# Kernel optimization log

Measured on AMD Instinct MI355X. Metric: run time of the kernel, lower is better.

The kernel has to match this reference:

```python
import jax, jax.numpy as jnp
import numpy as np

B, S, N, D, NAMED, NTYPES = 8, 64, 100, 1024, 768, 5

def _ln(x, g, b, eps=1e-5):
    m = x.mean(-1, keepdims=True)
    v = ((x - m) ** 2).mean(-1, keepdims=True)
    return (x - m) * jax.lax.rsqrt(v + eps) * g + b

def _lin(x, W, b=None):
    y = x @ W.T
    return y if b is None else y + b

def setup_inputs():
    key = jax.random.key(0)
    ks = jax.random.split(key, 24)
    p = lambda i, shape, s=0.02: jax.random.normal(ks[i], shape, jnp.float32) * s
    inp = {}
    inp['scene_reps'] = jax.random.normal(ks[0], (B, S, D), jnp.float32)
    u = jax.random.uniform(ks[1], (B, N, S))
    keep = (jax.random.uniform(ks[2], (B, N, S)) < 0.25).astype(jnp.float32)
    inp['incidence_matrix'] = u * keep
    inp['edge_type_ids'] = jax.random.randint(ks[3], (B, S), 0, NTYPES)
    inp['entity_type_ids'] = jax.random.randint(ks[4], (B, N), 0, NTYPES)
    inp['entity_mask'] = jax.random.uniform(ks[5], (B, N)) < 0.9
    inp['entity_name_embs'] = jax.random.normal(ks[6], (B, N, NAMED), jnp.float32)
    inp['type_embed'] = p(7, (NTYPES, D), 1.0)
    inp['name_W'] = p(8, (D, NAMED))
    inp['name_ln_g'] = jnp.ones(D); inp['name_ln_b'] = jnp.zeros(D)
    inp['n2e_W'] = p(9, (D, D)); inp['n2e_b'] = jnp.zeros(D)
    inp['t2e_W'] = p(10, (D, D)); inp['t2e_b'] = jnp.zeros(D)
    inp['edge_ln_g'] = jnp.ones(D); inp['edge_ln_b'] = jnp.zeros(D)
    inp['gate_W1'] = p(11, (D // 4, D)); inp['gate_b1'] = jnp.zeros(D // 4)
    inp['gate_W2'] = p(12, (3, D // 4)); inp['gate_b2'] = jnp.zeros(3)
    inp['ms_W'] = p(13, (D, D)); inp['ms_b'] = jnp.zeros(D)
    inp['ma_W'] = p(14, (D, D)); inp['ma_b'] = jnp.zeros(D)
    inp['mi_W'] = p(15, (D, D)); inp['mi_b'] = jnp.zeros(D)
    inp['role_w'] = p(16, (D,))
    inp['gru_Wih'] = p(17, (3 * D, D)); inp['gru_Whh'] = p(18, (3 * D, D))
    inp['gru_bih'] = jnp.zeros(3 * D); inp['gru_bhh'] = jnp.zeros(3 * D)
    inp['upd_ln_g'] = jnp.ones(D); inp['upd_ln_b'] = jnp.zeros(D)
    inp['eo_W'] = p(19, (D, D)); inp['eo_b'] = jnp.zeros(D)
    inp['eo_ln_g'] = jnp.ones(D); inp['eo_ln_b'] = jnp.zeros(D)
    inp['res_ln_g'] = jnp.ones(D); inp['res_ln_b'] = jnp.zeros(D)
    return inp

def reference(scene_reps, incidence_matrix, edge_type_ids, entity_type_ids, entity_mask, entity_name_embs, type_embed, name_W, name_ln_g, name_ln_b, n2e_W, n2e_b, t2e_W, t2e_b, edge_ln_g, edge_ln_b, gate_W1, gate_b1, gate_W2, gate_b2, ms_W, ms_b, ma_W, ma_b, mi_W, mi_b, role_w, gru_Wih, gru_Whh, gru_bih, gru_bhh, upd_ln_g, upd_ln_b, eo_W, eo_b, eo_ln_g, eo_ln_b, res_ln_g, res_ln_b):
    # edge_type_ids is accepted by the torch module but unused in its forward.
    dt = scene_reps.dtype
    emaskf = entity_mask.astype(dt)  # [B,N]
    h0 = type_embed[entity_type_ids] + _ln(_lin(entity_name_embs, name_W), name_ln_g, name_ln_b)
    h0 = h0 * emaskf[..., None]
    eye = jnp.eye(N, dtype=dt)
    step_ids = jnp.arange(S)

    def step(carry, xs):
        h, ebuf = carry  # h [B,N,D], ebuf [B,S,D] (hyperedge history)
        s, x_s, inc_s = xs  # x_s [B,D], inc_s [B,N]
        roles = inc_s * emaskf
        wsum = jnp.maximum(roles.sum(1, keepdims=True), 1.0)
        mean_ent = jnp.einsum('bn,bnd->bd', roles, h) / wsum
        e_s = _ln(_lin(mean_ent, n2e_W, n2e_b) + _lin(x_s, t2e_W, t2e_b), edge_ln_g, edge_ln_b)
        in_mask = (roles > 0).astype(dt)[..., None]  # [B,N,1]
        msg_scene = _lin(e_s, ms_W, ms_b)[:, None, :]
        # arc stream: attention over past hyperedges with exponential recency decay
        valid = (step_ids < s).astype(dt)
        denom = jnp.maximum(s - 1, 1).astype(dt)
        decay = jnp.exp(-1.0 + step_ids.astype(dt) / denom) * valid  # linspace(-1,0,s)
        arc = incidence_matrix * roles[:, :, None] * decay[None, None, :]  # [B,N,S]
        arc = arc / jnp.maximum(arc.sum(-1, keepdims=True), 1e-8)
        msg_arc = _lin(jnp.einsum('bns,bsd->bnd', arc, jax.lax.stop_gradient(ebuf)), ma_W, ma_b)
        msg_arc = jnp.where(s > 0, msg_arc, jnp.zeros_like(msg_arc))
        # interaction stream: entity co-occurrence within the scene
        co = roles[:, :, None] * roles[:, None, :] * (1.0 - eye)
        co = co / jnp.maximum(co.sum(-1, keepdims=True), 1e-8)
        msg_int = _lin(jnp.einsum('bnm,bmd->bnd', co, h), mi_W, mi_b)
        gate = jax.nn.softmax(_lin(jax.nn.gelu(_lin(e_s, gate_W1, gate_b1), approximate=False), gate_W2, gate_b2), axis=-1)  # [B,3]
        msg = gate[:, 0, None, None] * msg_scene + gate[:, 1, None, None] * msg_arc + gate[:, 2, None, None] * msg_int
        msg = msg + (roles[..., None] * role_w) * in_mask
        # GRUCell (torch semantics) + LayerNorm, masked update
        gi = _lin(msg, gru_Wih, gru_bih)
        gh = _lin(h, gru_Whh, gru_bhh)
        i_r, i_z, i_n = jnp.split(gi, 3, axis=-1)
        h_r, h_z, h_n = jnp.split(gh, 3, axis=-1)
        r = jax.nn.sigmoid(i_r + h_r)
        z = jax.nn.sigmoid(i_z + h_z)
        n = jnp.tanh(i_n + r * h_n)
        h_new = jnp.clip(_ln((1 - z) * n + z * h, upd_ln_g, upd_ln_b), -50.0, 50.0)
        h = h * (1 - in_mask) + h_new * in_mask
        ebuf = ebuf.at[:, s].set(e_s)
        return (h, ebuf), e_s

    ebuf0 = jnp.zeros((B, S, D), dt)
    (h_fin, _), es = jax.lax.scan(step, (h0, ebuf0), (step_ids, scene_reps.transpose(1, 0, 2), incidence_matrix.transpose(2, 0, 1)))
    H = es.transpose(1, 0, 2)  # [B,S,D]
    H = _ln(H + scene_reps, res_ln_g, res_ln_b)
    H = _ln(jax.nn.gelu(_lin(H, eo_W, eo_b), approximate=False), eo_ln_g, eo_ln_b)
    return (H, h_fin)
```

## Files before the change

kernel.cpp:

```cpp
#include <hip/hip_runtime.h>
#include <math.h>

#define B_   8
#define S_   64
#define N_   100
#define D_   1024
#define ND_  768
#define BN_  800
#define G3_  3072
#define G6_  6144
#define HC7  7168
#define RSC  0.00390625f

typedef _Float16 f16x8 __attribute__((ext_vector_type(8)));
typedef float f32x4 __attribute__((ext_vector_type(4)));

#define MFMA16(a,b,c) __builtin_amdgcn_mfma_f32_16x16x32_f16(a, b, c, 0, 0, 0)

static __device__ __forceinline__ float wave_sum(float v) {
    for (int off = 32; off > 0; off >>= 1) v += __shfl_down(v, off, 64);
    return v;
}

static __device__ __forceinline__ float wave_allsum(float v) {
    for (int off = 1; off < 64; off <<= 1) v += __shfl_xor(v, off, 64);
    return v;
}

static __device__ __forceinline__ float block_sum(float v) {
    __shared__ float red_[8];
    float w = wave_sum(v);
    int lane = threadIdx.x & 63, wid = threadIdx.x >> 6;
    __syncthreads();
    if (lane == 0) red_[wid] = w;
    __syncthreads();
    float t = 0.f;
    for (int i = 0; i < 4; ++i) t += red_[i];
    return t;
}

static __device__ __forceinline__ float gelu_f(float x) {
    return 0.5f * x * (1.f + erff(x * 0.70710678118654752f));
}

static __device__ __forceinline__ unsigned short f2h(float x) {
    union { _Float16 h; unsigned short u; } c; c.h = (_Float16)x; return c.u;
}

__global__ __launch_bounds__(256) void k_f2h(
    const float* __restrict__ src, unsigned short* __restrict__ dst,
    int rows, int cols, int ldd)
{
    size_t n = (size_t)rows * cols;
    size_t i = ((size_t)blockIdx.x * 256 + threadIdx.x) * 4;
    if (i >= n) return;
    int r = (int)(i / cols);
    int c = (int)(i - (size_t)r * cols);
    float4 v = *(const float4*)(src + i);
    ushort4 o; o.x = f2h(v.x); o.y = f2h(v.y); o.z = f2h(v.z); o.w = f2h(v.w);
    *(ushort4*)(dst + (size_t)r * ldd + c) = o;
}

__global__ __launch_bounds__(256) void k_f2hT(
    const float* __restrict__ src, unsigned short* __restrict__ dst,
    int R, int C, int ldd, int rowoff)
{
    __shared__ _Float16 T[32][33];
    int tr = threadIdx.x >> 3, tc4 = (threadIdx.x & 7) * 4;
    int r0 = blockIdx.y * 32, c0 = blockIdx.x * 32;
    float4 v = *(const float4*)(src + (size_t)(r0 + tr) * C + c0 + tc4);
    T[tc4][tr] = (_Float16)v.x; T[tc4+1][tr] = (_Float16)v.y;
    T[tc4+2][tr] = (_Float16)v.z; T[tc4+3][tr] = (_Float16)v.w;
    __syncthreads();
    union { _Float16 h; unsigned short u; } cv;
    ushort4 o;
    cv.h = T[tr][tc4];   o.x = cv.u;
    cv.h = T[tr][tc4+1]; o.y = cv.u;
    cv.h = T[tr][tc4+2]; o.z = cv.u;
    cv.h = T[tr][tc4+3]; o.w = cv.u;
    *(ushort4*)(dst + (size_t)(rowoff + c0 + tr) * ldd + r0 + tc4) = o;
}

__global__ __launch_bounds__(256) void k_mfma16_nt(
    const unsigned short* __restrict__ A16, const unsigned short* __restrict__ W16,
    const float* __restrict__ bias, float* __restrict__ C,
    unsigned short* __restrict__ C16, float oscale,
    int M, int Nc, int K)
{
    int m0 = blockIdx.y * 64; if (m0 >= M) return;
    int n0 = blockIdx.x * 128;
    __shared__ _Float16 sA[64][72];
    __shared__ _Float16 sB[128][72];
    int tid = threadIdx.x;
    int w = tid >> 6, l = tid & 63;
    int l15 = l & 15, q = l >> 4;
    int wn = w * 32;
    int arow = tid >> 3, achk = (tid & 7) * 8;
    f32x4 acc[4][2] = {};
    for (int k0 = 0; k0 < K; k0 += 64) {
        for (int ri = 0; ri < 64; ri += 32) {
            int gm = m0 + arow + ri;
            uint4 v = make_uint4(0u, 0u, 0u, 0u);
            if (gm < M) v = *(const uint4*)(A16 + (size_t)gm * K + k0 + achk);
            *(uint4*)(&sA[arow + ri][achk]) = v;
        }
        for (int i = 0; i < 4; ++i) {
            int r = arow + 32 * i;
            *(uint4*)(&sB[r][achk]) = *(const uint4*)(W16 + (size_t)(n0 + r) * K + k0 + achk);
        }
        __syncthreads();
#pragma unroll
        for (int ks = 0; ks < 64; ks += 32) {
            f16x8 b0 = *(const f16x8*)(&sB[wn + l15][ks + q*8]);
            f16x8 b1 = *(const f16x8*)(&sB[wn + 16 + l15][ks + q*8]);
#pragma unroll
            for (int mi = 0; mi < 4; ++mi) {
                f16x8 a = *(const f16x8*)(&sA[mi*16 + l15][ks + q*8]);
                acc[mi][0] = MFMA16(a, b0, acc[mi][0]);
                acc[mi][1] = MFMA16(a, b1, acc[mi][1]);
            }
        }
        __syncthreads();
    }
    for (int mi = 0; mi < 4; ++mi)
        for (int nj = 0; nj < 2; ++nj)
            for (int r = 0; r < 4; ++r) {
                int gm = m0 + mi*16 + q*4 + r;
                int cl = wn + nj*16 + l15;
                if (gm < M) {
                    size_t off = (size_t)gm * Nc + n0 + cl;
                    float v = acc[mi][nj][r];
                    if (C16) C16[off] = f2h(v * oscale);
                    else C[off] = v + (bias ? bias[n0 + cl] : 0.f);
                }
            }
}

__global__ __launch_bounds__(256) void k_h0(
    const float* __restrict__ P, const int* __restrict__ etype,
    const int* __restrict__ emask, const float* __restrict__ temb,
    const float* __restrict__ g, const float* __restrict__ bt,
    float* __restrict__ h, unsigned short* __restrict__ h16)
{
    int bn = blockIdx.x, tid = threadIdx.x;
    int t = etype[bn], mk = emask[bn];
    float x[4]; float lsum = 0.f;
    for (int k = 0; k < 4; ++k) { x[k] = P[(size_t)bn*D_ + tid + 256*k]; lsum += x[k]; }
    float mean = block_sum(lsum) * (1.f / D_);
    float lv = 0.f;
    for (int k = 0; k < 4; ++k) { float d = x[k] - mean; lv += d * d; }
    float inv = rsqrtf(block_sum(lv) * (1.f / D_) + 1e-5f);
    for (int k = 0; k < 4; ++k) {
        int d = tid + 256*k;
        float y = (x[k] - mean) * inv * g[d] + bt[d];
        float hv = mk ? (temb[(size_t)t*D_ + d] + y) : 0.f;
        h[(size_t)bn*D_ + d] = hv;
        h16[(size_t)bn*D_ + d] = f2h(hv);
    }
}

__global__ __launch_bounds__(256) void k_hcat0(
    const unsigned short* __restrict__ h16, const unsigned short* __restrict__ n2e16,
    const unsigned short* __restrict__ Wmi16, const unsigned short* __restrict__ Whh16,
    float* __restrict__ Hcat)
{
    int m0 = blockIdx.y * 32;
    int n0 = blockIdx.x * 64;
    const unsigned short* Bp; int ldb; int nl;
    if (n0 < 1024)      { Bp = n2e16;        ldb = D_;  nl = n0; }
    else if (n0 < 4096) { Bp = Wmi16 + 2048; ldb = G3_; nl = n0 - 1024; }
    else                { Bp = Whh16;        ldb = D_;  nl = n0 - 4096; }
    __shared__ _Float16 sA[32][72];
    __shared__ _Float16 sB[64][72];
    int tid = threadIdx.x;
    int w = tid >> 6, l = tid & 63;
    int l15 = l & 15, q = l >> 4;
    int wm = (w & 1) * 16, wn = (w >> 1) * 32;
    int arow = tid >> 3, achk = (tid & 7) * 8;
    int gmA = m0 + arow;
    f32x4 acc[2] = {};
    for (int k0 = 0; k0 < D_; k0 += 64) {
        *(uint4*)(&sA[arow][achk]) = *(const uint4*)(h16 + (size_t)gmA*D_ + k0 + achk);
        *(uint4*)(&sB[arow][achk])      = *(const uint4*)(Bp + (size_t)(nl + arow)*ldb + k0 + achk);
        *(uint4*)(&sB[arow + 32][achk]) = *(const uint4*)(Bp + (size_t)(nl + arow + 32)*ldb + k0 + achk);
        __syncthreads();
#pragma unroll
        for (int ks = 0; ks < 64; ks += 32) {
            f16x8 a  = *(const f16x8*)(&sA[wm + l15][ks + q*8]);
            f16x8 b0 = *(const f16x8*)(&sB[wn + l15][ks + q*8]);
            f16x8 b1 = *(const f16x8*)(&sB[wn + 16 + l15][ks + q*8]);
            acc[0] = MFMA16(a, b0, acc[0]);
            acc[1] = MFMA16(a, b1, acc[1]);
        }
        __syncthreads();
    }
    for (int j = 0; j < 2; ++j)
        for (int r = 0; r < 4; ++r) {
            int row = wm + q*4 + r;
            Hcat[(size_t)(m0 + row)*HC7 + n0 + wn + j*16 + l15] = acc[j][r];
        }
}

__global__ __launch_bounds__(256) void k_front(
    const float* __restrict__ inc, const int* __restrict__ emask,
    const float* __restrict__ Esmi, float* __restrict__ arcsum,
    int* __restrict__ cntp, int* __restrict__ lst, float* __restrict__ rro,
    float* __restrict__ scl,
    const int* __restrict__ prevcnt, const int* __restrict__ prevlist,
    const unsigned short* __restrict__ h16, const unsigned short* __restrict__ n2e16,
    const unsigned short* __restrict__ Wmi16, const unsigned short* __restrict__ Whh16,
    float* __restrict__ Hcat, float* __restrict__ gatepre,
    float* __restrict__ esumP, float* __restrict__ TmiP, float* __restrict__ wsumP,
    int s)
{
    int tid = threadIdx.x, bid = blockIdx.x;
    if (bid == 0 && tid < 32) gatepre[tid] = 0.f;
    if (bid < BN_) {
        int m = bid;
        int b = m / N_;
        float r = emask[m] ? inc[(size_t)m*S_ + s] : 0.f;
        if (r <= 0.f) return;
        __shared__ int sidx, nwa;
        __shared__ float wav[S_]; __shared__ int wai[S_];
        if (tid == 0) { sidx = atomicAdd(cntp, 1); nwa = 0; }
        __syncthreads();
        int idx = sidx;
        float denomA = fmaxf((float)(s - 1), 1.f);
        float wa = 0.f;
        if (tid < s) {
            float iv = inc[(size_t)m*S_ + tid];
            if (iv > 0.f) {
                wa = iv * r * expf(-1.f + (float)tid / denomA);
                int p = atomicAdd(&nwa, 1);
                wav[p] = wa; wai[p] = tid;
            }
        }
        float dA = block_sum(wa);
        float rm = 0.f;
        if (tid < N_) rm = emask[b*N_ + tid] ? inc[((size_t)b*N_ + tid)*S_ + s] : 0.f;
        float wsum = block_sum(rm);
        __syncthreads();
        int na = nwa;
        float sclA = 1.f / fmaxf(dA, 1e-8f);
        if (tid == 0) {
            lst[idx] = m; rro[idx] = r;
            scl[idx] = r / fmaxf(r * (wsum - r), 1e-8f);
            wsumP[b] = wsum;
        }
        float rprev = (s > 0) ? inc[(size_t)m*S_ + (s-1)] : 0.f;
        if (rprev <= 0.f) {
            const float4* hp = (const float4*)(Hcat + (size_t)m*HC7);
#pragma unroll
            for (int j2 = 0; j2 < 4; ++j2) {
                float4 hv = hp[tid + 256*j2];
                int c = (tid + 256*j2) * 4;
                float* dst = (c < 1024) ? (esumP + (size_t)b*D_ + c)
                                        : (TmiP + (size_t)b*G3_ + (c - 1024));
                atomicAdd(dst + 0, r*hv.x); atomicAdd(dst + 1, r*hv.y);
                atomicAdd(dst + 2, r*hv.z); atomicAdd(dst + 3, r*hv.w);
            }
        }
        float a12[12];
#pragma unroll
        for (int k = 0; k < 12; ++k) a12[k] = 0.f;
        for (int j = 0; j < na; ++j) {
            float wj = wav[j];
            const float* ep = Esmi + ((size_t)b*S_ + wai[j])*G3_;
#pragma unroll
            for (int k = 0; k < 12; ++k) a12[k] += wj * ep[tid + 256*k];
        }
        float* ao = arcsum + (size_t)idx*G3_;
#pragma unroll
        for (int k = 0; k < 12; ++k) ao[tid + 256*k] = a12[k] * sclA;
    } else {
        int pM = *prevcnt;
        int t = bid - BN_;
        int nt = t % 112, mt = t / 112;
        int m0 = mt * 64;
        if (m0 >= pM) return;
        int n0 = nt * 64;
        const unsigned short* Bp; int ldb; int nl;
        if (n0 < 1024)      { Bp = n2e16;        ldb = D_;  nl = n0; }
        else if (n0 < 4096) { Bp = Wmi16 + 2048; ldb = G3_; nl = n0 - 1024; }
        else                { Bp = Whh16;        ldb = D_;  nl = n0 - 4096; }
        __shared__ _Float16 sA[64][72];
        __shared__ _Float16 sB[64][72];
        __shared__ int slist[64];
        __shared__ float srn[64];
        __shared__ int sbb[64];
        if (tid < 64) {
            int gm = m0 + tid;
            int m = (gm < pM) ? prevlist[gm] : 0;
            slist[tid] = m;
            float rn = 0.f;
            if (gm < pM) rn = emask[m] ? inc[(size_t)m*S_ + s] : 0.f;
            srn[tid] = rn;
            sbb[tid] = m / N_;
        }
        __syncthreads();
        int w = tid >> 6, l = tid & 63;
        int l15 = l & 15, q = l >> 4;
        int wm = (w & 1) * 32, wn = (w >> 1) * 32;
        int arow = tid >> 3, achk = (tid & 7) * 8;
        f32x4 acc[2][2] = {};
        for (int k0 = 0; k0 < D_; k0 += 64) {
            for (int ri = 0; ri < 64; ri += 32) {
                int row = arow + ri, gm = m0 + row;
                uint4 v = make_uint4(0u,0u,0u,0u);
                if (gm < pM) v = *(const uint4*)(h16 + (size_t)slist[row]*D_ + k0 + achk);
                *(uint4*)(&sA[row][achk]) = v;
            }
            *(uint4*)(&sB[arow][achk])      = *(const uint4*)(Bp + (size_t)(nl + arow)*ldb + k0 + achk);
            *(uint4*)(&sB[arow + 32][achk]) = *(const uint4*)(Bp + (size_t)(nl + arow + 32)*ldb + k0 + achk);
            __syncthreads();
#pragma unroll
            for (int ks = 0; ks < 64; ks += 32) {
                f16x8 a0 = *(const f16x8*)(&sA[wm + l15][ks + q*8]);
                f16x8 a1 = *(const f16x8*)(&sA[wm + 16 + l15][ks + q*8]);
                f16x8 b0 = *(const f16x8*)(&sB[wn + l15][ks + q*8]);
                f16x8 b1 = *(const f16x8*)(&sB[wn + 16 + l15][ks + q*8]);
                acc[0][0] = MFMA16(a0, b0, acc[0][0]);
                acc[0][1] = MFMA16(a0, b1, acc[0][1]);
                acc[1][0] = MFMA16(a1, b0, acc[1][0]);
                acc[1][1] = MFMA16(a1, b1, acc[1][1]);
            }
            __syncthreads();
        }
        for (int mi = 0; mi < 2; ++mi)
            for (int nj = 0; nj < 2; ++nj)
                for (int r = 0; r < 4; ++r) {
                    int row = wm + mi*16 + q*4 + r;
                    int gm = m0 + row;
                    if (gm < pM) {
                        float v = acc[mi][nj][r];
                        int c = n0 + wn + nj*16 + l15;
                        Hcat[(size_t)slist[row]*HC7 + c] = v;
                        float rn = srn[row];
                        if (rn > 0.f && c < 4096) {
                            float* dst = (c < 1024)
                                ? (esumP + (size_t)sbb[row]*D_ + c)
                                : (TmiP + (size_t)sbb[row]*G3_ + (c - 1024));
                            atomicAdd(dst, rn * v);
                        }
                    }
                }
    }
}

__global__ __launch_bounds__(256) void k_mid(
    const float* __restrict__ esumP, const float* __restrict__ wsumP,
    float* __restrict__ esumZ, float* __restrict__ TmiZ, float* __restrict__ wsumZ,
    const float* __restrict__ n2eb, const float* __restrict__ pre_t2e,
    const float* __restrict__ elng, const float* __restrict__ elnb,
    const float* __restrict__ gW1, const float* __restrict__ gb1,
    const float* __restrict__ gW2, const unsigned short* __restrict__ Wmi16,
    float* __restrict__ esbuf, float* __restrict__ gatepre,
    float* __restrict__ Emi, float* __restrict__ Esmi,
    int* __restrict__ ctrl, int par, int s)
{
    int bid = blockIdx.x, tid = threadIdx.x;
    if (bid < 32) {
        __shared__ float se[D_];
        int b = bid >> 2, seg = bid & 3;
        if (bid == 0 && tid == 0) ctrl[1 - par] = 0;
        esumZ[(size_t)b*D_ + seg*256 + tid] = 0.f;
#pragma unroll
        for (int j = 0; j < 3; ++j) TmiZ[(size_t)b*G3_ + seg*768 + j*256 + tid] = 0.f;
        if (seg == 0 && tid == 0) wsumZ[b] = 0.f;
        float invw = 1.f / fmaxf(wsumP[b], 1.f);
        float4 ev = ((const float4*)(esumP + (size_t)b*D_))[tid];
        float4 nb = ((const float4*)n2eb)[tid];
        float4 pt = ((const float4*)(pre_t2e + ((size_t)b*S_ + s)*D_))[tid];
        float x[4] = { ev.x*invw + nb.x + pt.x, ev.y*invw + nb.y + pt.y,
                       ev.z*invw + nb.z + pt.z, ev.w*invw + nb.w + pt.w };
        float mean = block_sum(x[0]+x[1]+x[2]+x[3]) * (1.f / D_);
        float lv = 0.f;
#pragma unroll
        for (int k = 0; k < 4; ++k) { float d = x[k] - mean; lv += d * d; }
        float inv = rsqrtf(block_sum(lv) * (1.f / D_) + 1e-5f);
        float4 lg = ((const float4*)elng)[tid];
        float4 lb = ((const float4*)elnb)[tid];
        float y0 = (x[0]-mean)*inv*lg.x + lb.x;
        float y1 = (x[1]-mean)*inv*lg.y + lb.y;
        float y2 = (x[2]-mean)*inv*lg.z + lb.z;
        float y3 = (x[3]-mean)*inv*lg.w + lb.w;
        int d4 = tid * 4;
        se[d4] = y0; se[d4+1] = y1; se[d4+2] = y2; se[d4+3] = y3;
        if (seg == 0)
            ((float4*)(esbuf + ((size_t)b*S_ + s)*D_))[tid] = make_float4(y0,y1,y2,y3);
        __syncthreads();
        if (tid < 64) {
            int u = seg * 64 + tid;
            float acc = gb1[u];
            const float* w1 = gW1 + (size_t)u * D_;
            for (int j = 0; j < D_; j += 4) {
                float4 w = *(const float4*)(w1 + j);
                acc += w.x*se[j] + w.y*se[j+1] + w.z*se[j+2] + w.w*se[j+3];
            }
            float hg = gelu_f(acc);
            for (int c = 0; c < 3; ++c) {
                float p = wave_sum(gW2[c*256 + u] * hg);
                if (tid == 0) atomicAdd(gatepre + b*4 + c, p);
            }
        }
    } else {
        __shared__ float se32[8][1028];
        int w = tid >> 6, lane = tid & 63;
        for (int bb = 0; bb < 2; ++bb) {
            int b = w*2 + bb;
            float invw = 1.f / fmaxf(wsumP[b], 1.f);
            int d0 = lane * 16;
            const float4* ep = (const float4*)(esumP + (size_t)b*D_ + d0);
            const float4* np = (const float4*)(n2eb + d0);
            const float4* pp = (const float4*)(pre_t2e + ((size_t)b*S_ + s)*D_ + d0);
            float x[16]; float sm = 0.f;
#pragma unroll
            for (int j = 0; j < 4; ++j) {
                float4 e = ep[j], n = np[j], p = pp[j];
                x[j*4+0] = e.x*invw + n.x + p.x;
                x[j*4+1] = e.y*invw + n.y + p.y;
                x[j*4+2] = e.z*invw + n.z + p.z;
                x[j*4+3] = e.w*invw + n.w + p.w;
                sm += x[j*4+0] + x[j*4+1] + x[j*4+2] + x[j*4+3];
            }
            float mean = wave_allsum(sm) * (1.f / D_);
            float lv = 0.f;
#pragma unroll
            for (int j = 0; j < 16; ++j) { float d = x[j] - mean; lv += d * d; }
            float inv = rsqrtf(wave_allsum(lv) * (1.f / D_) + 1e-5f);
            const float4* lgp = (const float4*)(elng + d0);
            const float4* lbp = (const float4*)(elnb + d0);
#pragma unroll
            for (int j = 0; j < 4; ++j) {
                float4 lg = lgp[j], lb = lbp[j];
                se32[b][d0 + j*4 + 0] = (x[j*4+0]-mean)*inv*lg.x + lb.x;
                se32[b][d0 + j*4 + 1] = (x[j*4+1]-mean)*inv*lg.y + lb.y;
                se32[b][d0 + j*4 + 2] = (x[j*4+2]-mean)*inv*lg.z + lb.z;
                se32[b][d0 + j*4 + 3] = (x[j*4+3]-mean)*inv*lg.w + lb.w;
            }
        }
        __syncthreads();
        int c0 = (bid - 32) * 32;
        int colg = tid >> 5, t31 = tid & 31;
        int cb = c0 + colg * 4;
        float accA[4][8] = {};
        float accB[4][8] = {};
#pragma unroll
        for (int i = 0; i < 8; ++i) {
            int kh = t31*4 + i*128;
            float wf[4][4];
#pragma unroll
            for (int c = 0; c < 4; ++c) {
                union { uint2 u; _Float16 h[4]; } cv;
                cv.u = *(const uint2*)(Wmi16 + (size_t)(cb + c)*G3_ + kh);
                wf[c][0] = (float)cv.h[0]; wf[c][1] = (float)cv.h[1];
                wf[c][2] = (float)cv.h[2]; wf[c][3] = (float)cv.h[3];
            }
#pragma unroll
            for (int b = 0; b < 8; ++b) {
                float4 sv = *(const float4*)(&se32[b][kh]);
#pragma unroll
                for (int c = 0; c < 4; ++c)
                    accA[c][b] += wf[c][0]*sv.x + wf[c][1]*sv.y
                                + wf[c][2]*sv.z + wf[c][3]*sv.w;
            }
        }
#pragma unroll
        for (int i = 0; i < 8; ++i) {
            int kh = t31*4 + i*128;
            float wf[4][4];
#pragma unroll
            for (int c = 0; c < 4; ++c) {
                union { uint2 u; _Float16 h[4]; } cv;
                cv.u = *(const uint2*)(Wmi16 + (size_t)(cb + c)*G3_ + 1024 + kh);
                wf[c][0] = (float)cv.h[0]; wf[c][1] = (float)cv.h[1];
                wf[c][2] = (float)cv.h[2]; wf[c][3] = (float)cv.h[3];
            }
#pragma unroll
            for (int b = 0; b < 8; ++b) {
                float4 sv = *(const float4*)(&se32[b][kh]);
#pragma unroll
                for (int c = 0; c < 4; ++c)
                    accB[c][b] += wf[c][0]*sv.x + wf[c][1]*sv.y
                                + wf[c][2]*sv.z + wf[c][3]*sv.w;
            }
        }
#pragma unroll
        for (int off = 16; off >= 1; off >>= 1) {
#pragma unroll
            for (int c = 0; c < 4; ++c)
#pragma unroll
                for (int b = 0; b < 8; ++b) {
                    accA[c][b] += __shfl_down(accA[c][b], off, 32);
                    accB[c][b] += __shfl_down(accB[c][b], off, 32);
                }
        }
        if (t31 == 0) {
#pragma unroll
            for (int c = 0; c < 4; ++c) {
                int col = cb + c;
#pragma unroll
                for (int b = 0; b < 8; ++b) {
                    Emi[(size_t)b*G3_ + col] = accA[c][b];
                    Esmi[((size_t)b*S_ + s)*G3_ + col] = accB[c][b];
                }
            }
        }
    }
}

__global__ __launch_bounds__(256) void k_fin(
    const int* __restrict__ lst, const int* __restrict__ cntp,
    const float* __restrict__ rro, const float* __restrict__ scl,
    const float* __restrict__ gatepre, const float* __restrict__ gb2,
    const float* __restrict__ Hcat, const float* __restrict__ Emi,
    const float* __restrict__ arcsum, const float* __restrict__ Tmi,
    const float* __restrict__ gBm, const float* __restrict__ bih,
    const float* __restrict__ bhh,
    const float* __restrict__ ulng, const float* __restrict__ ulnb,
    float* __restrict__ h, unsigned short* __restrict__ h16, int s)
{
    int row = blockIdx.x;
    if (row >= *cntp) return;
    int bn = lst[row];
    int b = bn / N_;
    int tid = threadIdx.x;
    float t0 = gatepre[b*4+0] + gb2[0];
    float t1 = gatepre[b*4+1] + gb2[1];
    float t2 = gatepre[b*4+2] + gb2[2];
    float mx = fmaxf(t0, fmaxf(t1, t2));
    float e0 = expf(t0-mx), e1 = expf(t1-mx), e2 = expf(t2-mx);
    float si = 1.f / (e0 + e1 + e2);
    float g0 = e0*si, g1 = (s > 0) ? e1*si : 0.f, g2 = e2*si;
    float rv = rro[row];
    float sI = scl[row];
    const float* Hrow = Hcat + (size_t)bn * HC7;
    const float* em = Emi + (size_t)b * G3_;
    const float* as = arcsum + (size_t)row * G3_;
    const float* tm = Tmi + (size_t)b * G3_;
    float u[4]; float lsum = 0.f;
    for (int k = 0; k < 4; ++k) {
        int d = tid + 256*k;
        float ip[3];
#pragma unroll
        for (int c = 0; c < 3; ++c) {
            int dd = c*D_ + d;
            float gint = tm[dd] - rv * Hrow[1024 + dd];
            ip[c] = RSC * (g0*em[dd] + g1*as[dd] + g2*sI*gint)
                  + g0*gBm[dd] + g1*gBm[G3_ + dd] + g2*gBm[2*G3_ + dd]
                  + rv*gBm[3*G3_ + dd] + bih[dd];
        }
        float hr = Hrow[4096 + d]        + bhh[d];
        float hz = Hrow[4096 + D_ + d]   + bhh[D_ + d];
        float hn = Hrow[4096 + 2*D_ + d] + bhh[2*D_ + d];
        float hv = h[(size_t)bn*D_ + d];
        float r = 1.f / (1.f + expf(-(ip[0] + hr)));
        float z = 1.f / (1.f + expf(-(ip[1] + hz)));
        float nn = tanhf(ip[2] + r * hn);
        u[k] = (1.f - z) * nn + z * hv;
        lsum += u[k];
    }
    float mean = block_sum(lsum) * (1.f / D_);
    float lv = 0.f;
    for (int k = 0; k < 4; ++k) { float d = u[k] - mean; lv += d * d; }
    float inv = rsqrtf(block_sum(lv) * (1.f / D_) + 1e-5f);
    for (int k = 0; k < 4; ++k) {
        int d = tid + 256*k;
        float y = (u[k] - mean) * inv * ulng[d] + ulnb[d];
        y = fminf(fmaxf(y, -50.f), 50.f);
        h[(size_t)bn*D_ + d] = y;
        h16[(size_t)bn*D_ + d] = f2h(y);
    }
}

__global__ __launch_bounds__(256) void k_resln(
    float* __restrict__ buf, const float* __restrict__ scene,
    const float* __restrict__ g, const float* __restrict__ bt,
    unsigned short* __restrict__ H16)
{
    size_t row = blockIdx.x;
    int tid = threadIdx.x;
    float x[4]; float lsum = 0.f;
    for (int k = 0; k < 4; ++k) {
        int d = tid + 256*k;
        x[k] = buf[row*D_ + d] + scene[row*D_ + d];
        lsum += x[k];
    }
    float mean = block_sum(lsum) * (1.f / D_);
    float lv = 0.f;
    for (int k = 0; k < 4; ++k) { float d = x[k] - mean; lv += d * d; }
    float inv = rsqrtf(block_sum(lv) * (1.f / D_) + 1e-5f);
    for (int k = 0; k < 4; ++k) {
        int d = tid + 256*k;
        float y = (x[k] - mean) * inv * g[d] + bt[d];
        buf[row*D_ + d] = y;
        H16[row*D_ + d] = f2h(y);
    }
}

__global__ __launch_bounds__(256) void k_final(
    const float* __restrict__ G, const float* __restrict__ g, const float* __restrict__ bt,
    float* __restrict__ outH, const float* __restrict__ h, float* __restrict__ outh)
{
    int tid = threadIdx.x;
    if (blockIdx.x < B_*S_) {
        size_t row = blockIdx.x;
        float x[4]; float lsum = 0.f;
        for (int k = 0; k < 4; ++k) {
            x[k] = gelu_f(G[row*D_ + tid + 256*k]);
            lsum += x[k];
        }
        float mean = block_sum(lsum) * (1.f / D_);
        float lv = 0.f;
        for (int k = 0; k < 4; ++k) { float d = x[k] - mean; lv += d * d; }
        float inv = rsqrtf(block_sum(lv) * (1.f / D_) + 1e-5f);
        for (int k = 0; k < 4; ++k) {
            int d = tid + 256*k;
            outH[row*D_ + d] = (x[k] - mean) * inv * g[d] + bt[d];
        }
    } else {
        size_t bn = blockIdx.x - B_*S_;
        for (int d = tid; d < D_; d += 256)
            outh[bn*D_ + d] = h[bn*D_ + d];
    }
}

extern "C" void kernel_launch(void* const* d_in, const int* in_sizes, int n_in,
                              void* d_out, int out_size, void* d_ws, size_t ws_size,
                              hipStream_t stream)
{
    const float* scene = (const float*)d_in[0];
    const float* inc   = (const float*)d_in[1];
    const int*   etype = (const int*)d_in[3];
    const int*   emask = (const int*)d_in[4];
    const float* nemb  = (const float*)d_in[5];
    const float* temb  = (const float*)d_in[6];
    const float* nameW = (const float*)d_in[7];
    const float* nlg   = (const float*)d_in[8];
    const float* nlb   = (const float*)d_in[9];
    const float* n2eW  = (const float*)d_in[10];
    const float* n2eb  = (const float*)d_in[11];
    const float* t2eW  = (const float*)d_in[12];
    const float* t2eb  = (const float*)d_in[13];
    const float* elng  = (const float*)d_in[14];
    const float* elnb  = (const float*)d_in[15];
    const float* gW1   = (const float*)d_in[16];
    const float* gb1   = (const float*)d_in[17];
    const float* gW2   = (const float*)d_in[18];
    const float* gb2   = (const float*)d_in[19];
    const float* msW   = (const float*)d_in[20];
    const float* msB   = (const float*)d_in[21];
    const float* maW   = (const float*)d_in[22];
    const float* maB   = (const float*)d_in[23];
    const float* miW   = (const float*)d_in[24];
    const float* miB   = (const float*)d_in[25];
    const float* rolew = (const float*)d_in[26];
    const float* Wih   = (const float*)d_in[27];
    const float* Whh   = (const float*)d_in[28];
    const float* bih   = (const float*)d_in[29];
    const float* bhh   = (const float*)d_in[30];
    const float* ulng  = (const float*)d_in[31];
    const float* ulnb  = (const float*)d_in[32];
    const float* eoW   = (const float*)d_in[33];
    const float* eoB   = (const float*)d_in[34];
    const float* eolng = (const float*)d_in[35];
    const float* eolnb = (const float*)d_in[36];
    const float* rlng  = (const float*)d_in[37];
    const float* rlnb  = (const float*)d_in[38];

    float* outH = (float*)d_out;
    float* outh = outH + (size_t)B_*S_*D_;

    float* W = (float*)d_ws;
    size_t o = 0;
    int*   ctrl     = (int*)(W + o); o += 64;
    float* esum2    = W + o; o += 2*(size_t)B_*D_;
    float* Tmi2     = W + o; o += 2*(size_t)B_*G3_;
    float* wsum2    = W + o; o += 16;
    float* gatepre  = W + o; o += 32;
    float* rowrole  = W + o; o += 2*BN_;
    float* sclbuf   = W + o; o += BN_;
    int*   list     = (int*)(W + o); o += 2*BN_;
    float* hbuf     = W + o; o += (size_t)BN_*D_;
    float* Hcat     = W + o; o += (size_t)BN_*HC7;
    float* pre_t2e  = W + o; o += (size_t)B_*S_*D_;
    float* gBm      = W + o; o += 4*G3_;
    float* Emi      = W + o; o += (size_t)B_*G3_;
    float* Esmi     = W + o; o += (size_t)B_*S_*G3_;
    float* arcsum   = W + o; o += (size_t)BN_*G3_;
    float* tmp      = W + o; o += (size_t)BN_*D_;
    unsigned short* U = (unsigned short*)(W + o);
    size_t uo = 0;
    unsigned short* h16    = U + uo; uo += (size_t)BN_*D_;
    unsigned short* H16    = U + uo; uo += (size_t)B_*S_*D_;
    unsigned short* Wih16  = U + uo; uo += (size_t)G3_*D_;
    unsigned short* Whh16  = U + uo; uo += (size_t)G3_*D_;
    unsigned short* n2e16  = U + uo; uo += (size_t)D_*D_;
    unsigned short* eoW16  = U + uo; uo += (size_t)D_*D_;
    unsigned short* nW16   = U + uo; uo += (size_t)D_*ND_;
    unsigned short* nE16   = U + uo; uo += (size_t)BN_*ND_;
    unsigned short* t2e16  = U + uo; uo += (size_t)D_*D_;
    unsigned short* sc16   = U + uo; uo += (size_t)B_*S_*D_;
    unsigned short* WcatT16= U + uo; uo += (size_t)G3_*D_;
    unsigned short* Wmi16  = U + uo; uo += (size_t)G3_*G3_;
    unsigned short* bias4  = U + uo; uo += 4*D_;

    hipMemsetAsync(ctrl, 0,
        (64 + 2*(size_t)B_*D_ + 2*(size_t)B_*G3_ + 16) * sizeof(float), stream);

    #define CVT(src, dst, r, c, ld) \
        k_f2h<<<(((size_t)(r)*(c)/4 + 255)/256), 256, 0, stream>>>(src, dst, r, c, ld)
    CVT(Wih,   Wih16, G3_, D_,  D_);
    CVT(Whh,   Whh16, G3_, D_,  D_);
    CVT(n2eW,  n2e16, D_,  D_,  D_);
    CVT(nameW, nW16,  D_,  ND_, ND_);
    CVT(nemb,  nE16,  BN_, ND_, ND_);
    CVT(eoW,   eoW16, D_,  D_,  D_);
    CVT(t2eW,  t2e16, D_,  D_,  D_);
    CVT(scene, sc16,  B_*S_, D_, D_);
    CVT(msB,   bias4 + 0,    1, D_, D_);
    CVT(maB,   bias4 + D_,   1, D_, D_);
    CVT(miB,   bias4 + 2*D_, 1, D_, D_);
    CVT(rolew, bias4 + 3*D_, 1, D_, D_);
    #undef CVT
    k_f2hT<<<dim3(32,32), 256, 0, stream>>>(msW, WcatT16, D_, D_, D_, 0);
    k_f2hT<<<dim3(32,32), 256, 0, stream>>>(maW, WcatT16, D_, D_, D_, D_);
    k_f2hT<<<dim3(32,32), 256, 0, stream>>>(miW, WcatT16, D_, D_, D_, 2*D_);

    k_mfma16_nt<<<dim3(G3_/128, G3_/64), 256, 0, stream>>>(
        Wih16, WcatT16, nullptr, nullptr, Wmi16, 256.f, G3_, G3_, D_);
    k_mfma16_nt<<<dim3(G3_/128, 1), 256, 0, stream>>>(
        bias4, Wih16, nullptr, gBm, nullptr, 1.f, 4, G3_, D_);
    k_mfma16_nt<<<dim3(D_/128, (B_*S_+63)/64), 256, 0, stream>>>(
        sc16, t2e16, t2eb, pre_t2e, nullptr, 1.f, B_*S_, D_, D_);
    k_mfma16_nt<<<dim3(D_/128, (BN_+63)/64), 256, 0, stream>>>(
        nE16, nW16, nullptr, tmp, nullptr, 1.f, BN_, D_, ND_);
    k_h0<<<BN_, 256, 0, stream>>>(tmp, etype, emask, temb, nlg, nlb, hbuf, h16);
    k_hcat0<<<dim3(112, 25), 256, 0, stream>>>(h16, n2e16, Wmi16, Whh16, Hcat);

    for (int s = 0; s < S_; ++s) {
        int par = s & 1;
        int*   cntp = ctrl + par;
        int*   pcnt = ctrl + (1 - par);
        int*   lst  = list + par * BN_;
        int*   plst = list + (1 - par) * BN_;
        float* rro  = rowrole + par * BN_;
        float* esumP = esum2 + (size_t)par * B_*D_;
        float* esumZ = esum2 + (size_t)(1 - par) * B_*D_;
        float* TmiP  = Tmi2 + (size_t)par * B_*G3_;
        float* TmiZ  = Tmi2 + (size_t)(1 - par) * B_*G3_;
        float* wsumP = wsum2 + par * 8;
        float* wsumZ = wsum2 + (1 - par) * 8;
        k_front<<<BN_ + 112*13, 256, 0, stream>>>(inc, emask, Esmi, arcsum,
            cntp, lst, rro, sclbuf, pcnt, plst, h16, n2e16, Wmi16, Whh16,
            Hcat, gatepre, esumP, TmiP, wsumP, s);
        k_mid<<<128, 256, 0, stream>>>(esumP, wsumP, esumZ, TmiZ, wsumZ,
            n2eb, pre_t2e, elng, elnb, gW1, gb1, gW2, Wmi16,
            outH, gatepre, Emi, Esmi, ctrl, par, s);
        k_fin<<<BN_, 256, 0, stream>>>(lst, cntp, rro, sclbuf, gatepre, gb2,
            Hcat, Emi, arcsum, TmiP, gBm, bih, bhh, ulng, ulnb, hbuf, h16, s);
    }

    k_resln<<<B_*S_, 256, 0, stream>>>(outH, scene, rlng, rlnb, H16);
    k_mfma16_nt<<<dim3(D_/128, (B_*S_+63)/64), 256, 0, stream>>>(
        H16, eoW16, eoB, tmp, nullptr, 1.f, B_*S_, D_, D_);
    k_final<<<B_*S_ + BN_, 256, 0, stream>>>(tmp, eolng, eolnb, outH, hbuf, outh);
}
```

Before: 4.203 ms.

## Fuse per-step recurrent kernels into one persistent cooperative kernel with grid syncs

Replaces the 64-step loop of three kernel launches (front, mid, fin) with a single persistent cooperative kernel that loops over steps. Each former kernel becomes a phase, and grid.sync() separates the phases. The grid is capped at 512 blocks, and each block strides over that phase's tasks. The aim is to remove about 192 kernel launches and their launch gaps. In exchange, occupancy and parallelism per phase are limited to the co-resident grid, and grid-wide barrier costs are added. If cooperative launch fails, the code falls back to the original multi-launch loop.

```diff
diff --git a/kernel.cpp b/kernel.cpp
--- a/kernel.cpp
+++ b/kernel.cpp
@@ -1,4 +1,5 @@
 #include <hip/hip_runtime.h>
+#include <hip/hip_cooperative_groups.h>
 #include <math.h>
 
 #define B_   8
@@ -8,12 +9,14 @@
 #define ND_  768
 #define BN_  800
 #define G3_  3072
-#define G6_  6144
 #define HC7  7168
+#define NBLK 512
 #define RSC  0.00390625f
 
 typedef _Float16 f16x8 __attribute__((ext_vector_type(8)));
 typedef float f32x4 __attribute__((ext_vector_type(4)));
+
+namespace cg = cooperative_groups;
 
 #define MFMA16(a,b,c) __builtin_amdgcn_mfma_f32_16x16x32_f16(a, b, c, 0, 0, 0)
 
@@ -570,6 +573,394 @@
         y = fminf(fmaxf(y, -50.f), 50.f);
         h[(size_t)bn*D_ + d] = y;
         h16[(size_t)bn*D_ + d] = f2h(y);
+    }
+}
+
+struct LoopA {
+    const float* inc; const int* emask;
+    float* Esmi; float* arcsum;
+    int* ctrl; int* list2; float* rro2; float* scl;
+    unsigned short* h16; float* hbuf;
+    const unsigned short* n2e16; const unsigned short* Wmi16; const unsigned short* Whh16;
+    float* Hcat; float* gatepre;
+    float* esum2; float* Tmi2; float* wsum2;
+    const float* pre_t2e; float* Emi; float* esbuf;
+    const float* n2eb; const float* elng; const float* elnb;
+    const float* gW1; const float* gb1; const float* gW2; const float* gb2;
+    const float* gBm; const float* bih; const float* bhh;
+    const float* ulng; const float* ulnb;
+};
+
+union SMu {
+    struct { _Float16 A[64][72]; _Float16 Bm[64][72]; int slist[64]; float srn[64]; int sbb[64]; } g;
+    struct { float se32[8][1028]; } e;
+    struct { float se1[D_]; } t;
+    struct { float wav[S_]; int wai[S_]; } r;
+};
+
+__global__ __launch_bounds__(256, 2) void k_loop(LoopA a)
+{
+    cg::grid_group grid = cg::this_grid();
+    __shared__ SMu sm;
+    __shared__ int sh_i0, sh_i1;
+    int tid = threadIdx.x;
+    int bid = blockIdx.x;
+    int gdim = gridDim.x;
+
+    for (int s = 0; s < S_; ++s) {
+        int par = s & 1;
+        int* cntp = a.ctrl + par;
+        const int* pcnt = a.ctrl + (1 - par);
+        int* lst = a.list2 + par * BN_;
+        const int* plst = a.list2 + (1 - par) * BN_;
+        float* rro = a.rro2 + par * BN_;
+        float* esumP = a.esum2 + (size_t)par * B_ * D_;
+        float* esumZ = a.esum2 + (size_t)(1 - par) * B_ * D_;
+        float* TmiP  = a.Tmi2 + (size_t)par * B_ * G3_;
+        float* TmiZ  = a.Tmi2 + (size_t)(1 - par) * B_ * G3_;
+        const float* wsumP = a.wsum2 + par * 8;
+        float* wsumPw = a.wsum2 + par * 8;
+        float* wsumZ = a.wsum2 + (1 - par) * 8;
+
+        for (int tk = bid; tk < BN_ + 112*13; tk += gdim) {
+            __syncthreads();
+            if (tk < BN_) {
+                if (tk == 0 && tid < 32) a.gatepre[tid] = 0.f;
+                int m = tk, b = m / N_;
+                float r = a.emask[m] ? a.inc[(size_t)m*S_ + s] : 0.f;
+                if (r > 0.f) {
+                    if (tid == 0) { sh_i0 = atomicAdd(cntp, 1); sh_i1 = 0; }
+                    __syncthreads();
+                    int idx = sh_i0;
+                    float denomA = fmaxf((float)(s - 1), 1.f);
+                    float wa = 0.f;
+                    if (tid < s) {
+                        float iv = a.inc[(size_t)m*S_ + tid];
+                        if (iv > 0.f) {
+                            wa = iv * r * expf(-1.f + (float)tid / denomA);
+                            int p = atomicAdd(&sh_i1, 1);
+                            sm.r.wav[p] = wa; sm.r.wai[p] = tid;
+                        }
+                    }
+                    float dA = block_sum(wa);
+                    float rm = 0.f;
+                    if (tid < N_) rm = a.emask[b*N_ + tid] ? a.inc[((size_t)b*N_ + tid)*S_ + s] : 0.f;
+                    float wsum = block_sum(rm);
+                    __syncthreads();
+                    int na = sh_i1;
+                    float sclA = 1.f / fmaxf(dA, 1e-8f);
+                    if (tid == 0) {
+                        lst[idx] = m; rro[idx] = r;
+                        a.scl[idx] = r / fmaxf(r * (wsum - r), 1e-8f);
+                        wsumPw[b] = wsum;
+                    }
+                    float rprev = (s > 0) ? a.inc[(size_t)m*S_ + (s-1)] : 0.f;
+                    if (rprev <= 0.f) {
+                        const float4* hp = (const float4*)(a.Hcat + (size_t)m*HC7);
+#pragma unroll
+                        for (int j2 = 0; j2 < 4; ++j2) {
+                            float4 hv = hp[tid + 256*j2];
+                            int c = (tid + 256*j2) * 4;
+                            float* dst = (c < 1024) ? (esumP + (size_t)b*D_ + c)
+                                                    : (TmiP + (size_t)b*G3_ + (c - 1024));
+                            atomicAdd(dst + 0, r*hv.x); atomicAdd(dst + 1, r*hv.y);
+                            atomicAdd(dst + 2, r*hv.z); atomicAdd(dst + 3, r*hv.w);
+                        }
+                    }
+                    float a12[12];
+#pragma unroll
+                    for (int k = 0; k < 12; ++k) a12[k] = 0.f;
+                    for (int j = 0; j < na; ++j) {
+                        float wj = sm.r.wav[j];
+                        const float* ep = a.Esmi + ((size_t)b*S_ + sm.r.wai[j])*G3_;
+#pragma unroll
+                        for (int k = 0; k < 12; ++k) a12[k] += wj * ep[tid + 256*k];
+                    }
+                    float* ao = a.arcsum + (size_t)idx*G3_;
+#pragma unroll
+                    for (int k = 0; k < 12; ++k) ao[tid + 256*k] = a12[k] * sclA;
+                }
+            } else {
+                int pM = *pcnt;
+                int t = tk - BN_;
+                int nt = t % 112, mt = t / 112;
+                int m0 = mt * 64;
+                if (m0 < pM) {
+                    int n0 = nt * 64;
+                    const unsigned short* Bp; int ldb; int nl;
+                    if (n0 < 1024)      { Bp = a.n2e16;        ldb = D_;  nl = n0; }
+                    else if (n0 < 4096) { Bp = a.Wmi16 + 2048; ldb = G3_; nl = n0 - 1024; }
+                    else                { Bp = a.Whh16;        ldb = D_;  nl = n0 - 4096; }
+                    if (tid < 64) {
+                        int gm = m0 + tid;
+                        int m = (gm < pM) ? plst[gm] : 0;
+                        sm.g.slist[tid] = m;
+                        float rn = 0.f;
+                        if (gm < pM) rn = a.emask[m] ? a.inc[(size_t)m*S_ + s] : 0.f;
+                        sm.g.srn[tid] = rn;
+                        sm.g.sbb[tid] = m / N_;
+                    }
+                    __syncthreads();
+                    int w = tid >> 6, l = tid & 63;
+                    int l15 = l & 15, q = l >> 4;
+                    int wm = (w & 1) * 32, wn = (w >> 1) * 32;
+                    int arow = tid >> 3, achk = (tid & 7) * 8;
+                    f32x4 acc[2][2] = {};
+                    for (int k0 = 0; k0 < D_; k0 += 64) {
+                        for (int ri = 0; ri < 64; ri += 32) {
+                            int row = arow + ri, gm = m0 + row;
+                            uint4 v = make_uint4(0u,0u,0u,0u);
+                            if (gm < pM) v = *(const uint4*)(a.h16 + (size_t)sm.g.slist[row]*D_ + k0 + achk);
+                            *(uint4*)(&sm.g.A[row][achk]) = v;
+                        }
+                        *(uint4*)(&sm.g.Bm[arow][achk])      = *(const uint4*)(Bp + (size_t)(nl + arow)*ldb + k0 + achk);
+                        *(uint4*)(&sm.g.Bm[arow + 32][achk]) = *(const uint4*)(Bp + (size_t)(nl + arow + 32)*ldb + k0 + achk);
+                        __syncthreads();
+#pragma unroll
+                        for (int ks = 0; ks < 64; ks += 32) {
+                            f16x8 a0 = *(const f16x8*)(&sm.g.A[wm + l15][ks + q*8]);
+                            f16x8 a1 = *(const f16x8*)(&sm.g.A[wm + 16 + l15][ks + q*8]);
+                            f16x8 b0 = *(const f16x8*)(&sm.g.Bm[wn + l15][ks + q*8]);
+                            f16x8 b1 = *(const f16x8*)(&sm.g.Bm[wn + 16 + l15][ks + q*8]);
+                            acc[0][0] = MFMA16(a0, b0, acc[0][0]);
+                            acc[0][1] = MFMA16(a0, b1, acc[0][1]);
+                            acc[1][0] = MFMA16(a1, b0, acc[1][0]);
+                            acc[1][1] = MFMA16(a1, b1, acc[1][1]);
+                        }
+                        __syncthreads();
+                    }
+                    for (int mi = 0; mi < 2; ++mi)
+                        for (int nj = 0; nj < 2; ++nj)
+                            for (int r4 = 0; r4 < 4; ++r4) {
+                                int row = wm + mi*16 + q*4 + r4;
+                                int gm = m0 + row;
+                                if (gm < pM) {
+                                    float v = acc[mi][nj][r4];
+                                    int c = n0 + wn + nj*16 + l15;
+                                    a.Hcat[(size_t)sm.g.slist[row]*HC7 + c] = v;
+                                    float rn = sm.g.srn[row];
+                                    if (rn > 0.f && c < 4096) {
+                                        float* dst = (c < 1024)
+                                            ? (esumP + (size_t)sm.g.sbb[row]*D_ + c)
+                                            : (TmiP + (size_t)sm.g.sbb[row]*G3_ + (c - 1024));
+                                        atomicAdd(dst, rn * v);
+                                    }
+                                }
+                            }
+                }
+            }
+        }
+        grid.sync();
+
+        for (int tk = bid; tk < 128; tk += gdim) {
+            __syncthreads();
+            if (tk < 32) {
+                int b = tk >> 2, seg = tk & 3;
+                if (tk == 0 && tid == 0) a.ctrl[1 - par] = 0;
+                esumZ[(size_t)b*D_ + seg*256 + tid] = 0.f;
+#pragma unroll
+                for (int j = 0; j < 3; ++j) TmiZ[(size_t)b*G3_ + seg*768 + j*256 + tid] = 0.f;
+                if (seg == 0 && tid == 0) wsumZ[b] = 0.f;
+                float invw = 1.f / fmaxf(wsumP[b], 1.f);
+                float4 ev = ((const float4*)(esumP + (size_t)b*D_))[tid];
+                float4 nb = ((const float4*)a.n2eb)[tid];
+                float4 pt = ((const float4*)(a.pre_t2e + ((size_t)b*S_ + s)*D_))[tid];
+                float x[4] = { ev.x*invw + nb.x + pt.x, ev.y*invw + nb.y + pt.y,
+                               ev.z*invw + nb.z + pt.z, ev.w*invw + nb.w + pt.w };
+                float mean = block_sum(x[0]+x[1]+x[2]+x[3]) * (1.f / D_);
+                float lv = 0.f;
+#pragma unroll
+                for (int k = 0; k < 4; ++k) { float d = x[k] - mean; lv += d * d; }
+                float inv = rsqrtf(block_sum(lv) * (1.f / D_) + 1e-5f);
+                float4 lg = ((const float4*)a.elng)[tid];
+                float4 lb = ((const float4*)a.elnb)[tid];
+                float y0 = (x[0]-mean)*inv*lg.x + lb.x;
+                float y1 = (x[1]-mean)*inv*lg.y + lb.y;
+                float y2 = (x[2]-mean)*inv*lg.z + lb.z;
+                float y3 = (x[3]-mean)*inv*lg.w + lb.w;
+                int d4 = tid * 4;
+                sm.t.se1[d4] = y0; sm.t.se1[d4+1] = y1;
+                sm.t.se1[d4+2] = y2; sm.t.se1[d4+3] = y3;
+                if (seg == 0)
+                    ((float4*)(a.esbuf + ((size_t)b*S_ + s)*D_))[tid] = make_float4(y0,y1,y2,y3);
+                __syncthreads();
+                if (tid < 64) {
+                    int u = seg * 64 + tid;
+                    float acc = a.gb1[u];
+                    const float* w1 = a.gW1 + (size_t)u * D_;
+                    for (int j = 0; j < D_; j += 4) {
+                        float4 w = *(const float4*)(w1 + j);
+                        acc += w.x*sm.t.se1[j] + w.y*sm.t.se1[j+1] + w.z*sm.t.se1[j+2] + w.w*sm.t.se1[j+3];
+                    }
+                    float hg = gelu_f(acc);
+                    for (int c = 0; c < 3; ++c) {
+                        float p = wave_sum(a.gW2[c*256 + u] * hg);
+                        if (tid == 0) atomicAdd(a.gatepre + b*4 + c, p);
+                    }
+                }
+            } else {
+                int w = tid >> 6, lane = tid & 63;
+                for (int bb = 0; bb < 2; ++bb) {
+                    int b = w*2 + bb;
+                    float invw = 1.f / fmaxf(wsumP[b], 1.f);
+                    int d0 = lane * 16;
+                    const float4* ep = (const float4*)(esumP + (size_t)b*D_ + d0);
+                    const float4* np = (const float4*)(a.n2eb + d0);
+                    const float4* pp = (const float4*)(a.pre_t2e + ((size_t)b*S_ + s)*D_ + d0);
+                    float x[16]; float smv = 0.f;
+#pragma unroll
+                    for (int j = 0; j < 4; ++j) {
+                        float4 e = ep[j], n = np[j], p = pp[j];
+                        x[j*4+0] = e.x*invw + n.x + p.x;
+                        x[j*4+1] = e.y*invw + n.y + p.y;
+                        x[j*4+2] = e.z*invw + n.z + p.z;
+                        x[j*4+3] = e.w*invw + n.w + p.w;
+                        smv += x[j*4+0] + x[j*4+1] + x[j*4+2] + x[j*4+3];
+                    }
+                    float mean = wave_allsum(smv) * (1.f / D_);
+                    float lv = 0.f;
+#pragma unroll
+                    for (int j = 0; j < 16; ++j) { float d = x[j] - mean; lv += d * d; }
+                    float inv = rsqrtf(wave_allsum(lv) * (1.f / D_) + 1e-5f);
+                    const float4* lgp = (const float4*)(a.elng + d0);
+                    const float4* lbp = (const float4*)(a.elnb + d0);
+#pragma unroll
+                    for (int j = 0; j < 4; ++j) {
+                        float4 lg = lgp[j], lb = lbp[j];
+                        sm.e.se32[b][d0 + j*4 + 0] = (x[j*4+0]-mean)*inv*lg.x + lb.x;
+                        sm.e.se32[b][d0 + j*4 + 1] = (x[j*4+1]-mean)*inv*lg.y + lb.y;
+                        sm.e.se32[b][d0 + j*4 + 2] = (x[j*4+2]-mean)*inv*lg.z + lb.z;
+                        sm.e.se32[b][d0 + j*4 + 3] = (x[j*4+3]-mean)*inv*lg.w + lb.w;
+                    }
+                }
+                __syncthreads();
+                int c0 = (tk - 32) * 32;
+                int colg = tid >> 5, t31 = tid & 31;
+                int cb = c0 + colg * 4;
+                float accA[4][8] = {};
+                float accB[4][8] = {};
+#pragma unroll
+                for (int i = 0; i < 8; ++i) {
+                    int kh = t31*4 + i*128;
+                    float wf[4][4];
+#pragma unroll
+                    for (int c = 0; c < 4; ++c) {
+                        union { uint2 u; _Float16 hh[4]; } cv;
+                        cv.u = *(const uint2*)(a.Wmi16 + (size_t)(cb + c)*G3_ + kh);
+                        wf[c][0] = (float)cv.hh[0]; wf[c][1] = (float)cv.hh[1];
+                        wf[c][2] = (float)cv.hh[2]; wf[c][3] = (float)cv.hh[3];
+                    }
+#pragma unroll
+                    for (int b = 0; b < 8; ++b) {
+                        float4 sv = *(const float4*)(&sm.e.se32[b][kh]);
+#pragma unroll
+                        for (int c = 0; c < 4; ++c)
+                            accA[c][b] += wf[c][0]*sv.x + wf[c][1]*sv.y
+                                        + wf[c][2]*sv.z + wf[c][3]*sv.w;
+                    }
+                }
+#pragma unroll
+                for (int i = 0; i < 8; ++i) {
+                    int kh = t31*4 + i*128;
+                    float wf[4][4];
+#pragma unroll
+                    for (int c = 0; c < 4; ++c) {
+                        union { uint2 u; _Float16 hh[4]; } cv;
+                        cv.u = *(const uint2*)(a.Wmi16 + (size_t)(cb + c)*G3_ + 1024 + kh);
+                        wf[c][0] = (float)cv.hh[0]; wf[c][1] = (float)cv.hh[1];
+                        wf[c][2] = (float)cv.hh[2]; wf[c][3] = (float)cv.hh[3];
+                    }
+#pragma unroll
+                    for (int b = 0; b < 8; ++b) {
+                        float4 sv = *(const float4*)(&sm.e.se32[b][kh]);
+#pragma unroll
+                        for (int c = 0; c < 4; ++c)
+                            accB[c][b] += wf[c][0]*sv.x + wf[c][1]*sv.y
+                                        + wf[c][2]*sv.z + wf[c][3]*sv.w;
+                    }
+                }
+#pragma unroll
+                for (int off = 16; off >= 1; off >>= 1) {
+#pragma unroll
+                    for (int c = 0; c < 4; ++c)
+#pragma unroll
+                        for (int b = 0; b < 8; ++b) {
+                            accA[c][b] += __shfl_down(accA[c][b], off, 32);
+                            accB[c][b] += __shfl_down(accB[c][b], off, 32);
+                        }
+                }
+                if (t31 == 0) {
+#pragma unroll
+                    for (int c = 0; c < 4; ++c) {
+                        int col = cb + c;
+#pragma unroll
+                        for (int b = 0; b < 8; ++b) {
+                            a.Emi[(size_t)b*G3_ + col] = accA[c][b];
+                            a.Esmi[((size_t)b*S_ + s)*G3_ + col] = accB[c][b];
+                        }
+                    }
+                }
+            }
+        }
+        grid.sync();
+
+        {
+            int cnt = *cntp;
+            for (int tk = bid; tk < BN_; tk += gdim) {
+                __syncthreads();
+                if (tk >= cnt) continue;
+                int row = tk;
+                int bn = lst[row];
+                int b = bn / N_;
+                float t0 = a.gatepre[b*4+0] + a.gb2[0];
+                float t1 = a.gatepre[b*4+1] + a.gb2[1];
+                float t2 = a.gatepre[b*4+2] + a.gb2[2];
+                float mx = fmaxf(t0, fmaxf(t1, t2));
+                float e0 = expf(t0-mx), e1 = expf(t1-mx), e2 = expf(t2-mx);
+                float si = 1.f / (e0 + e1 + e2);
+                float g0 = e0*si, g1 = (s > 0) ? e1*si : 0.f, g2 = e2*si;
+                float rv = rro[row];
+                float sI = a.scl[row];
+                const float* Hrow = a.Hcat + (size_t)bn * HC7;
+                const float* em = a.Emi + (size_t)b * G3_;
+                const float* as = a.arcsum + (size_t)row * G3_;
+                const float* tm = TmiP + (size_t)b * G3_;
+                float u4[4]; float lsum = 0.f;
+                for (int k = 0; k < 4; ++k) {
+                    int d = tid + 256*k;
+                    float ip[3];
+#pragma unroll
+                    for (int c = 0; c < 3; ++c) {
+                        int dd = c*D_ + d;
+                        float gint = tm[dd] - rv * Hrow[1024 + dd];
+                        ip[c] = RSC * (g0*em[dd] + g1*as[dd] + g2*sI*gint)
+                              + g0*a.gBm[dd] + g1*a.gBm[G3_ + dd] + g2*a.gBm[2*G3_ + dd]
+                              + rv*a.gBm[3*G3_ + dd] + a.bih[dd];
+                    }
+                    float hr = Hrow[4096 + d]        + a.bhh[d];
+                    float hz = Hrow[4096 + D_ + d]   + a.bhh[D_ + d];
+                    float hn = Hrow[4096 + 2*D_ + d] + a.bhh[2*D_ + d];
+                    float hv = a.hbuf[(size_t)bn*D_ + d];
+                    float r = 1.f / (1.f + expf(-(ip[0] + hr)));
+                    float z = 1.f / (1.f + expf(-(ip[1] + hz)));
+                    float nn = tanhf(ip[2] + r * hn);
+                    u4[k] = (1.f - z) * nn + z * hv;
+                    lsum += u4[k];
+                }
+                float mean = block_sum(lsum) * (1.f / D_);
+                float lv = 0.f;
+                for (int k = 0; k < 4; ++k) { float d = u4[k] - mean; lv += d * d; }
+                float inv = rsqrtf(block_sum(lv) * (1.f / D_) + 1e-5f);
+                for (int k = 0; k < 4; ++k) {
+                    int d = tid + 256*k;
+                    float y = (u4[k] - mean) * inv * a.ulng[d] + a.ulnb[d];
+                    y = fminf(fmaxf(y, -50.f), 50.f);
+                    a.hbuf[(size_t)bn*D_ + d] = y;
+                    a.h16[(size_t)bn*D_ + d] = f2h(y);
+                }
+            }
+        }
+        grid.sync();
     }
 }
 
@@ -738,27 +1129,58 @@
     k_h0<<<BN_, 256, 0, stream>>>(tmp, etype, emask, temb, nlg, nlb, hbuf, h16);
     k_hcat0<<<dim3(112, 25), 256, 0, stream>>>(h16, n2e16, Wmi16, Whh16, Hcat);
 
-    for (int s = 0; s < S_; ++s) {
-        int par = s & 1;
-        int*   cntp = ctrl + par;
-        int*   pcnt = ctrl + (1 - par);
-        int*   lst  = list + par * BN_;
-        int*   plst = list + (1 - par) * BN_;
-        float* rro  = rowrole + par * BN_;
-        float* esumP = esum2 + (size_t)par * B_*D_;
-        float* esumZ = esum2 + (size_t)(1 - par) * B_*D_;
-        float* TmiP  = Tmi2 + (size_t)par * B_*G3_;
-        float* TmiZ  = Tmi2 + (size_t)(1 - par) * B_*G3_;
-        float* wsumP = wsum2 + par * 8;
-        float* wsumZ = wsum2 + (1 - par) * 8;
-        k_front<<<BN_ + 112*13, 256, 0, stream>>>(inc, emask, Esmi, arcsum,
-            cntp, lst, rro, sclbuf, pcnt, plst, h16, n2e16, Wmi16, Whh16,
-            Hcat, gatepre, esumP, TmiP, wsumP, s);
-        k_mid<<<128, 256, 0, stream>>>(esumP, wsumP, esumZ, TmiZ, wsumZ,
-            n2eb, pre_t2e, elng, elnb, gW1, gb1, gW2, Wmi16,
-            outH, gatepre, Emi, Esmi, ctrl, par, s);
-        k_fin<<<BN_, 256, 0, stream>>>(lst, cntp, rro, sclbuf, gatepre, gb2,
-            Hcat, Emi, arcsum, TmiP, gBm, bih, bhh, ulng, ulnb, hbuf, h16, s);
+    int dev = 0, coopAttr = 0, nCU = 0, mb = 0;
+    hipGetDevice(&dev);
+    hipDeviceGetAttribute(&coopAttr, hipDeviceAttributeCooperativeLaunch, dev);
+    hipDeviceGetAttribute(&nCU, hipDeviceAttributeMultiprocessorCount, dev);
+    hipOccupancyMaxActiveBlocksPerMultiprocessor(&mb, (const void*)k_loop, 256, 0);
+    int coopGrid = 0;
+    if (coopAttr && mb > 0 && nCU > 0) {
+        long cap = (long)mb * nCU;
+        coopGrid = (int)(cap < NBLK ? cap : NBLK);
+    }
+    hipError_t cerr = hipErrorUnknown;
+    if (coopGrid >= 64) {
+        LoopA la;
+        la.inc = inc; la.emask = emask;
+        la.Esmi = Esmi; la.arcsum = arcsum;
+        la.ctrl = ctrl; la.list2 = list; la.rro2 = rowrole; la.scl = sclbuf;
+        la.h16 = h16; la.hbuf = hbuf;
+        la.n2e16 = n2e16; la.Wmi16 = Wmi16; la.Whh16 = Whh16;
+        la.Hcat = Hcat; la.gatepre = gatepre;
+        la.esum2 = esum2; la.Tmi2 = Tmi2; la.wsum2 = wsum2;
+        la.pre_t2e = pre_t2e; la.Emi = Emi; la.esbuf = outH;
+        la.n2eb = n2eb; la.elng = elng; la.elnb = elnb;
+        la.gW1 = gW1; la.gb1 = gb1; la.gW2 = gW2; la.gb2 = gb2;
+        la.gBm = gBm; la.bih = bih; la.bhh = bhh;
+        la.ulng = ulng; la.ulnb = ulnb;
+        void* kargs[] = { (void*)&la };
+        cerr = hipLaunchCooperativeKernel((const void*)k_loop, dim3(coopGrid),
+                                          dim3(256), kargs, 0, stream);
+    }
+    if (cerr != hipSuccess) {
+        for (int s = 0; s < S_; ++s) {
+            int par = s & 1;
+            int*   cntp = ctrl + par;
+            int*   pcnt = ctrl + (1 - par);
+            int*   lst  = list + par * BN_;
+            int*   plst = list + (1 - par) * BN_;
+            float* rro  = rowrole + par * BN_;
+            float* esumP = esum2 + (size_t)par * B_*D_;
+            float* esumZ = esum2 + (size_t)(1 - par) * B_*D_;
+            float* TmiP  = Tmi2 + (size_t)par * B_*G3_;
+            float* TmiZ  = Tmi2 + (size_t)(1 - par) * B_*G3_;
+            float* wsumP = wsum2 + par * 8;
+            float* wsumZ = wsum2 + (1 - par) * 8;
+            k_front<<<BN_ + 112*13, 256, 0, stream>>>(inc, emask, Esmi, arcsum,
+                cntp, lst, rro, sclbuf, pcnt, plst, h16, n2e16, Wmi16, Whh16,
+                Hcat, gatepre, esumP, TmiP, wsumP, s);
+            k_mid<<<128, 256, 0, stream>>>(esumP, wsumP, esumZ, TmiZ, wsumZ,
+                n2eb, pre_t2e, elng, elnb, gW1, gb1, gW2, Wmi16,
+                outH, gatepre, Emi, Esmi, ctrl, par, s);
+            k_fin<<<BN_, 256, 0, stream>>>(lst, cntp, rro, sclbuf, gatepre, gb2,
+                Hcat, Emi, arcsum, TmiP, gBm, bih, bhh, ulng, ulnb, hbuf, h16, s);
+        }
     }
 
     k_resln<<<B_*S_, 256, 0, stream>>>(outH, scene, rlng, rlnb, H16);
```

New measurement: 14.13 ms. 3.36x slower.
